# Kernel optimization log

Hardware: AMD Instinct MI355X
Metric: run time of the kernel (lower is better)

## Reference

```python
import jax, jax.numpy as jnp
import numpy as np

L, B, D, H = 2048, 2, 1024, 16
HD = D // H
DFF = 4 * D
EPS = 1e-5


def layernorm(x, g, b):
    mu = jnp.mean(x, axis=-1, keepdims=True)
    var = jnp.mean((x - mu) ** 2, axis=-1, keepdims=True)
    return (x - mu) * jax.lax.rsqrt(var + EPS) * g + b


def setup_inputs() -> dict:
    key = jax.random.key(0)
    ks = jax.random.split(key, 12)
    s = 0.02
    return {
        "x": jax.random.normal(ks[0], (L, B, D), jnp.float32),
        "ln1_g": jnp.ones((D,), jnp.float32),
        "ln1_b": jnp.zeros((D,), jnp.float32),
        "w_attn": jax.random.normal(ks[1], (D, 3 * D), jnp.float32) * s,
        "b_attn": jnp.zeros((3 * D,), jnp.float32),
        "w_proj": jax.random.normal(ks[2], (D, D), jnp.float32) * s,
        "b_proj": jnp.zeros((D,), jnp.float32),
        "ln2_g": jnp.ones((D,), jnp.float32),
        "ln2_b": jnp.zeros((D,), jnp.float32),
        "w_fc": jax.random.normal(ks[3], (D, DFF), jnp.float32) * s,
        "b_fc": jnp.zeros((DFF,), jnp.float32),
        "w_out": jax.random.normal(ks[4], (DFF, D), jnp.float32) * s,
        "b_out": jnp.zeros((D,), jnp.float32),
    }


def reference(x, ln1_g, ln1_b, w_attn, b_attn, w_proj, b_proj,
              ln2_g, ln2_b, w_fc, b_fc, w_out, b_out):
    # x: [L, B, D]
    h = layernorm(x, ln1_g, ln1_b)
    qkv = h @ w_attn + b_attn                     # [L, B, 3D]
    qkv = jnp.transpose(qkv, (1, 0, 2))            # [B, L, 3D]
    q, k, v = jnp.split(qkv, 3, axis=-1)

    def split_heads(t):                            # [B, L, D] -> [B, H, L, hd]
        return jnp.transpose(t.reshape(B, L, H, HD), (0, 2, 1, 3))

    q, k, v = split_heads(q), split_heads(k), split_heads(v)
    # present: stack of (key, value), key in [B,H,L,hd] layout (post transpose-back)
    present = jnp.stack((k, v))                    # [2, B, H, L, hd]

    scores = jnp.einsum('bhqd,bhkd->bhqk', q, k) / jnp.sqrt(jnp.float32(HD))
    w = jax.nn.softmax(scores, axis=-1)
    a = jnp.einsum('bhqk,bhkd->bhqd', w, v)        # [B, H, L, hd]
    a = jnp.transpose(a, (0, 2, 1, 3)).reshape(B, L, D)
    a = a @ w_proj + b_proj                        # [B, L, D]
    a = jnp.transpose(a, (1, 0, 2))                # [L, B, D]

    x = x + a
    m = jax.nn.gelu(layernorm(x, ln2_g, ln2_b) @ w_fc + b_fc) @ w_out + b_out
    x = x + m
    return x, present
```

## Files before the change

kernel.cpp:

```cpp
#include <hip/hip_runtime.h>
#include <stdint.h>

#define L_SEQ 2048
#define BATCH 2
#define DIM   1024
#define NH    16
#define HDIM  64
#define DFF_  4096
#define ROWS  (L_SEQ*BATCH)

#define QSCALE 0.18033688011112042f

typedef __attribute__((ext_vector_type(8))) short  bf16x8;
typedef __attribute__((ext_vector_type(4))) float  floatx4;

__device__ __forceinline__ unsigned short f2bf(float f) {
    union { float f; uint32_t u; } x; x.f = f;
    uint32_t r = x.u + 0x7fffu + ((x.u >> 16) & 1u);
    return (unsigned short)(r >> 16);
}
__device__ __forceinline__ float bf2f(unsigned short b) {
    union { uint32_t u; float f; } x; x.u = ((uint32_t)b) << 16;
    return x.f;
}
__device__ __forceinline__ uint32_t fbits(float f) {
    union { float f; uint32_t u; } x; x.f = f; return x.u;
}

__device__ __forceinline__ void load_lds16(const unsigned short* g, unsigned short* l) {
    __builtin_amdgcn_global_load_lds(
        (const __attribute__((address_space(1))) unsigned int*)g,
        (__attribute__((address_space(3))) unsigned int*)l, 16, 0, 0);
}

__global__ __launch_bounds__(256)
void transpose_all(const float* __restrict__ s0, unsigned short* __restrict__ d0,
                   const float* __restrict__ s1, unsigned short* __restrict__ d1,
                   const float* __restrict__ s2, unsigned short* __restrict__ d2,
                   const float* __restrict__ s3, unsigned short* __restrict__ d3)
{
    const int id = blockIdx.x;
    const float* src; unsigned short* dst; int K, N, local;
    if (id < 3072)      { src = s0; dst = d0; K = 1024; N = 3072; local = id; }
    else if (id < 4096) { src = s1; dst = d1; K = 1024; N = 1024; local = id - 3072; }
    else if (id < 8192) { src = s2; dst = d2; K = 1024; N = 4096; local = id - 4096; }
    else                { src = s3; dst = d3; K = 4096; N = 1024; local = id - 8192; }
    const int nN = N >> 5;
    const int bk = (local / nN) * 32, bn = (local % nN) * 32;

    __shared__ float tile[32][36];
    const int t = threadIdx.x;
    const int r = t >> 3, c4 = (t & 7) * 4;
    *(float4*)&tile[r][c4] = *(const float4*)(src + (size_t)(bk + r) * N + bn + c4);
    __syncthreads();
    ushort4 o;
    o.x = f2bf(tile[c4 + 0][r]);
    o.y = f2bf(tile[c4 + 1][r]);
    o.z = f2bf(tile[c4 + 2][r]);
    o.w = f2bf(tile[c4 + 3][r]);
    *(ushort4*)(dst + (size_t)(bn + r) * K + bk + c4) = o;
}

template<int INBF16>
__global__ __launch_bounds__(256)
void ln_rows(const void* __restrict__ xin, const float* __restrict__ g,
             const float* __restrict__ bta, unsigned short* __restrict__ out)
{
    const int row = blockIdx.x;
    const int t = threadIdx.x;
    float4 v;
    if (INBF16) {
        const ushort4 u = ((const ushort4*)((const unsigned short*)xin + (size_t)row * DIM))[t];
        v.x = bf2f(u.x); v.y = bf2f(u.y); v.z = bf2f(u.z); v.w = bf2f(u.w);
    } else {
        v = ((const float4*)((const float*)xin + (size_t)row * DIM))[t];
    }
    float s  = v.x + v.y + v.z + v.w;
    float s2 = v.x*v.x + v.y*v.y + v.z*v.z + v.w*v.w;
#pragma unroll
    for (int d = 1; d < 64; d <<= 1) { s += __shfl_xor(s, d, 64); s2 += __shfl_xor(s2, d, 64); }
    __shared__ float ss[4], ss2[4];
    const int w = t >> 6, lane = t & 63;
    if (lane == 0) { ss[w] = s; ss2[w] = s2; }
    __syncthreads();
    s  = ss[0] + ss[1] + ss[2] + ss[3];
    s2 = ss2[0] + ss2[1] + ss2[2] + ss2[3];
    const float mu   = s * (1.0f / DIM);
    const float var  = s2 * (1.0f / DIM) - mu * mu;
    const float rstd = rsqrtf(var + 1e-5f);
    const float4 gv = ((const float4*)g)[t];
    const float4 bv = ((const float4*)bta)[t];
    ushort4 o;
    o.x = f2bf((v.x - mu) * rstd * gv.x + bv.x);
    o.y = f2bf((v.y - mu) * rstd * gv.y + bv.y);
    o.z = f2bf((v.z - mu) * rstd * gv.z + bv.z);
    o.w = f2bf((v.w - mu) * rstd * gv.w + bv.w);
    *(ushort4*)(out + (size_t)row * DIM + t * 4) = o;
}

template<int GELU, int RESID, int OUTBF16, int MI>
__global__ __launch_bounds__(256)
void gemm_bt(const unsigned short* __restrict__ A,
             const unsigned short* __restrict__ Bt,
             const float* __restrict__ bias,
             const void* __restrict__ resid,
             void* __restrict__ outp,
             int M, int N, int K)
{
    __shared__ unsigned short As[MI * 32 * 32];
    __shared__ unsigned short Bs[128 * 32];
    const int t = threadIdx.x;
    const int w = t >> 6, lane = t & 63;
    const int quad = lane >> 4, l16 = lane & 15;
    const int wm = (w >> 1) * (MI * 16), wn = (w & 1) * 64;
    const int bm = blockIdx.x * (MI * 32), bn = blockIdx.y * 128;

    const int srow = lane >> 2;
    const int scol = (lane & 3) * 8;

    const unsigned short* Ab = A  + (size_t)bm * K;
    const unsigned short* Bb = Bt + (size_t)bn * K;

    floatx4 acc[MI][4] = {};

    for (int kc = 0; kc < K; kc += 32) {
        __syncthreads();
#pragma unroll
        for (int i = 0; i < MI / 2; ++i) {
            const int r0 = (i * 4 + w) * 16;
            load_lds16(Ab + (size_t)(r0 + srow) * K + kc + scol, As + r0 * 32);
        }
#pragma unroll
        for (int i = 0; i < 2; ++i) {
            const int r0 = (i * 4 + w) * 16;
            load_lds16(Bb + (size_t)(r0 + srow) * K + kc + scol, Bs + r0 * 32);
        }
        __syncthreads();
        bf16x8 af[MI], bf[4];
#pragma unroll
        for (int i = 0; i < MI; ++i) af[i] = *(const bf16x8*)(As + (wm + i*16 + l16) * 32 + quad * 8);
#pragma unroll
        for (int j = 0; j < 4; ++j) bf[j] = *(const bf16x8*)(Bs + (wn + j*16 + l16) * 32 + quad * 8);
#pragma unroll
        for (int i = 0; i < MI; ++i)
#pragma unroll
            for (int j = 0; j < 4; ++j)
                acc[i][j] = __builtin_amdgcn_mfma_f32_16x16x32_bf16(af[i], bf[j], acc[i][j], 0, 0, 0);
    }

#pragma unroll
    for (int i = 0; i < MI; ++i) {
#pragma unroll
        for (int j = 0; j < 4; ++j) {
            const int col = bn + wn + j*16 + l16;
            const float bv = bias[col];
#pragma unroll
            for (int r = 0; r < 4; ++r) {
                const int row = bm + wm + i*16 + quad*4 + r;
                float v = acc[i][j][r] + bv;
                if (RESID == 1) v += ((const float*)resid)[(size_t)row * N + col];
                if (RESID == 2) v += bf2f(((const unsigned short*)resid)[(size_t)row * N + col]);
                if (GELU) {
                    const float u = v;
                    float c = 2.302204225929898f * (u + 0.044715f * u * u * u);
                    c = fminf(c, 80.f);
                    const float e = exp2f(c);
                    v = u * (e / (1.0f + e));
                }
                if (OUTBF16) ((unsigned short*)outp)[(size_t)row * N + col] = f2bf(v);
                else         ((float*)outp)[(size_t)row * N + col] = v;
            }
        }
    }
}

__global__ __launch_bounds__(256)
void split_qkv(const unsigned short* __restrict__ qkv,
               unsigned short* __restrict__ q, unsigned short* __restrict__ k,
               float* __restrict__ present)
{
    const size_t idx = (size_t)blockIdx.x * 256 + threadIdx.x;
    const int g8  = idx & 7;
    const int l   = (idx >> 3) & 2047;
    const int bh  = (idx >> 14) & 31;
    const int sel = (int)(idx >> 19);
    const int b = bh >> 4, h = bh & 15;
    const unsigned short* src = qkv + (size_t)(l * BATCH + b) * (3 * DIM) + sel * DIM + h * HDIM + g8 * 8;
    const uint4 val = *(const uint4*)src;
    const unsigned short* sv = (const unsigned short*)&val;
    if (sel == 0) {
        unsigned short ov[8];
#pragma unroll
        for (int j = 0; j < 8; ++j) ov[j] = f2bf(bf2f(sv[j]) * QSCALE);
        *(uint4*)(q + ((size_t)bh * L_SEQ + l) * HDIM + g8 * 8) = *(uint4*)ov;
    } else {
        *(uint4*)(k + ((size_t)bh * L_SEQ + l) * HDIM + g8 * 8) = val;
        float* p = present + (((size_t)b * NH + h) * L_SEQ + l) * HDIM + (size_t)g8 * 8;
        float4 f0, f1;
        f0.x = bf2f(sv[0]); f0.y = bf2f(sv[1]); f0.z = bf2f(sv[2]); f0.w = bf2f(sv[3]);
        f1.x = bf2f(sv[4]); f1.y = bf2f(sv[5]); f1.z = bf2f(sv[6]); f1.w = bf2f(sv[7]);
        ((float4*)p)[0] = f0; ((float4*)p)[1] = f1;
    }
}

__global__ __launch_bounds__(256)
void transpose_v(const unsigned short* __restrict__ qkv, unsigned short* __restrict__ vt,
                 float* __restrict__ present)
{
    __shared__ unsigned short tile[64][72];
    const int lt = blockIdx.x;
    const int bh = blockIdx.y;
    const int b = bh >> 4, h = bh & 15;
    const int t = threadIdx.x;
#pragma unroll
    for (int i = 0; i < 2; ++i) {
        const int idx = i * 256 + t;
        const int l = idx >> 3, c = (idx & 7) * 8;
        const uint4 val =
            *(const uint4*)(qkv + (size_t)((lt * 64 + l) * BATCH + b) * (3 * DIM) + 2 * DIM + h * HDIM + c);
        *(uint4*)(&tile[l][c]) = val;
        const unsigned short* sv = (const unsigned short*)&val;
        float* p = present + ((((size_t)BATCH + b) * NH + h) * L_SEQ + lt * 64 + l) * HDIM + c;
        float4 f0, f1;
        f0.x = bf2f(sv[0]); f0.y = bf2f(sv[1]); f0.z = bf2f(sv[2]); f0.w = bf2f(sv[3]);
        f1.x = bf2f(sv[4]); f1.y = bf2f(sv[5]); f1.z = bf2f(sv[6]); f1.w = bf2f(sv[7]);
        ((float4*)p)[0] = f0; ((float4*)p)[1] = f1;
    }
    __syncthreads();
#pragma unroll
    for (int i = 0; i < 2; ++i) {
        const int idx = i * 256 + t;
        const int d = idx >> 3, l0 = (idx & 7) * 8;
        const int kk = l0 >> 3;
        ushort4 o[2];
        unsigned short* ov = (unsigned short*)o;
#pragma unroll
        for (int jj = 0; jj < 8; ++jj) {
            const int j = (jj + kk) & 7;
            ov[j] = tile[l0 + j][d];
        }
        *(uint4*)(vt + ((size_t)bh * HDIM + d) * L_SEQ + lt * 64 + l0) = *(uint4*)o;
    }
}

__global__ __launch_bounds__(256, 4)
void attn_kernel(const unsigned short* __restrict__ Q,
                 const unsigned short* __restrict__ Kk,
                 const unsigned short* __restrict__ Vt,
                 unsigned short* __restrict__ Opart,
                 float* __restrict__ Lpart)
{
    const int qt = blockIdx.x;
    const int ks = blockIdx.y;
    const int bh = blockIdx.z;
    const int b = bh >> 4, h = bh & 15;
    const int t = threadIdx.x, w = t >> 6, lane = t & 63;
    const int quad = lane >> 4, l16 = lane & 15;

    __shared__ unsigned short Ks[64][72];
    __shared__ unsigned short Vts[64][72];
    __shared__ unsigned short Ps[4][32][72];

    const size_t head_off = (size_t)bh * L_SEQ * HDIM;
    const int q_base = qt * 128 + w * 32;
    const int kt0 = ks * 1024;

    bf16x8 qf[2][2];
#pragma unroll
    for (int nf = 0; nf < 2; ++nf)
#pragma unroll
        for (int ds = 0; ds < 2; ++ds)
            qf[nf][ds] = *(const bf16x8*)(Q + head_off + (size_t)(q_base + nf*16 + l16) * HDIM + ds*32 + quad*8);

    const int sr = t >> 3;
    const int sc = (t & 7) * 8;

    floatx4 o[4][2] = {};
    float l_i[2] = {0.f, 0.f};

    for (int kt = kt0; kt < kt0 + 1024; kt += 64) {
        __syncthreads();
#pragma unroll
        for (int i = 0; i < 2; ++i) {
            const int row = sr + i * 32;
            *(uint4*)(&Ks[row][sc])  = *(const uint4*)(Kk + head_off + (size_t)(kt + row) * HDIM + sc);
            *(uint4*)(&Vts[row][sc]) = *(const uint4*)(Vt + head_off + (size_t)row * L_SEQ + kt + sc);
        }
        __syncthreads();

        floatx4 s[4][2] = {};
#pragma unroll
        for (int ds = 0; ds < 2; ++ds)
#pragma unroll
            for (int jt = 0; jt < 4; ++jt) {
                const bf16x8 kf = *(const bf16x8*)(&Ks[jt*16 + l16][ds*32 + quad*8]);
                s[jt][0] = __builtin_amdgcn_mfma_f32_16x16x32_bf16(kf, qf[0][ds], s[jt][0], 0, 0, 0);
                s[jt][1] = __builtin_amdgcn_mfma_f32_16x16x32_bf16(kf, qf[1][ds], s[jt][1], 0, 0, 0);
            }

#pragma unroll
        for (int nf = 0; nf < 2; ++nf)
#pragma unroll
            for (int jt = 0; jt < 4; ++jt) {
                const float p0 = exp2f(s[jt][nf][0]);
                const float p1 = exp2f(s[jt][nf][1]);
                const float p2 = exp2f(s[jt][nf][2]);
                const float p3 = exp2f(s[jt][nf][3]);
                l_i[nf] += (p0 + p1) + (p2 + p3);
                uint2 pk;
                pk.x = __builtin_amdgcn_perm(fbits(p1), fbits(p0), 0x07060302u);
                pk.y = __builtin_amdgcn_perm(fbits(p3), fbits(p2), 0x07060302u);
                *(uint2*)(&Ps[w][nf*16 + l16][jt*16 + quad*4]) = pk;
            }

#pragma unroll
        for (int kk = 0; kk < 2; ++kk) {
            const bf16x8 pf0 = *(const bf16x8*)(&Ps[w][l16]     [kk*32 + quad*8]);
            const bf16x8 pf1 = *(const bf16x8*)(&Ps[w][16 + l16][kk*32 + quad*8]);
#pragma unroll
            for (int dt = 0; dt < 4; ++dt) {
                const bf16x8 vf = *(const bf16x8*)(&Vts[dt*16 + l16][kk*32 + quad*8]);
                o[dt][0] = __builtin_amdgcn_mfma_f32_16x16x32_bf16(vf, pf0, o[dt][0], 0, 0, 0);
                o[dt][1] = __builtin_amdgcn_mfma_f32_16x16x32_bf16(vf, pf1, o[dt][1], 0, 0, 0);
            }
        }
    }

    unsigned short* Op = Opart + (size_t)ks * ROWS * DIM;
#pragma unroll
    for (int nf = 0; nf < 2; ++nf) {
        float l = l_i[nf];
        l += __shfl_xor(l, 16, 64);
        l += __shfl_xor(l, 32, 64);
        const int q = q_base + nf*16 + l16;
        if (quad == 0)
            Lpart[((size_t)ks * 32 + bh) * L_SEQ + q] = l;
#pragma unroll
        for (int dt = 0; dt < 4; ++dt) {
            ushort4 ov;
            ov.x = f2bf(o[dt][nf][0]); ov.y = f2bf(o[dt][nf][1]);
            ov.z = f2bf(o[dt][nf][2]); ov.w = f2bf(o[dt][nf][3]);
            *(ushort4*)(Op + (size_t)(q * BATCH + b) * DIM + h * HDIM + dt*16 + quad*4) = ov;
        }
    }
}

__global__ __launch_bounds__(256)
void attn_merge(const unsigned short* __restrict__ Opart,
                const float* __restrict__ Lpart,
                unsigned short* __restrict__ Aout)
{
    const int row = blockIdx.x;
    const int q = row >> 1, b = row & 1;
    const int t = threadIdx.x;
    const int col = t * 4;
    const int h = col >> 6;
    const int bh = b * 16 + h;
    const float l0 = Lpart[(size_t)bh * L_SEQ + q];
    const float l1 = Lpart[((size_t)32 + bh) * L_SEQ + q];
    const float inv = 1.0f / (l0 + l1);
    const ushort4 o0 = *(const ushort4*)(Opart + (size_t)row * DIM + col);
    const ushort4 o1 = *(const ushort4*)(Opart + (size_t)ROWS * DIM + (size_t)row * DIM + col);
    ushort4 ov;
    ov.x = f2bf((bf2f(o0.x) + bf2f(o1.x)) * inv);
    ov.y = f2bf((bf2f(o0.y) + bf2f(o1.y)) * inv);
    ov.z = f2bf((bf2f(o0.z) + bf2f(o1.z)) * inv);
    ov.w = f2bf((bf2f(o0.w) + bf2f(o1.w)) * inv);
    *(ushort4*)(Aout + (size_t)row * DIM + col) = ov;
}

extern "C" void kernel_launch(void* const* d_in, const int* in_sizes, int n_in,
                              void* d_out, int out_size, void* d_ws, size_t ws_size,
                              hipStream_t stream)
{
    const float* x      = (const float*)d_in[0];
    const float* ln1_g  = (const float*)d_in[1];
    const float* ln1_b  = (const float*)d_in[2];
    const float* w_attn = (const float*)d_in[3];
    const float* b_attn = (const float*)d_in[4];
    const float* w_proj = (const float*)d_in[5];
    const float* b_proj = (const float*)d_in[6];
    const float* ln2_g  = (const float*)d_in[7];
    const float* ln2_b  = (const float*)d_in[8];
    const float* w_fc   = (const float*)d_in[9];
    const float* b_fc   = (const float*)d_in[10];
    const float* w_out  = (const float*)d_in[11];
    const float* b_out  = (const float*)d_in[12];

    char* ws = (char*)d_ws;
    unsigned short* watT   = (unsigned short*)(ws + 0);
    unsigned short* wprojT = (unsigned short*)(ws + 6291456);
    unsigned short* wfcT   = (unsigned short*)(ws + 8388608);
    unsigned short* woutT  = (unsigned short*)(ws + 16777216);
    unsigned short* h      = (unsigned short*)(ws + 25165824);
    unsigned short* qkv    = (unsigned short*)(ws + 33554432);
    unsigned short* opart  = (unsigned short*)(ws + 33554432);
    float*          lpart  = (float*)(ws + 50331648);
    unsigned short* mws    = (unsigned short*)(ws + 33554432);
    unsigned short* qw     = (unsigned short*)(ws + 58720256);
    unsigned short* kw     = (unsigned short*)(ws + 67108864);
    unsigned short* vt     = (unsigned short*)(ws + 75497472);
    unsigned short* aw     = (unsigned short*)(ws + 83886080);
    unsigned short* x2     = (unsigned short*)(ws + 92274688);

    float* xout    = (float*)d_out;
    float* present = (float*)d_out + 4194304;

    transpose_all<<<12288, 256, 0, stream>>>(w_attn, watT, w_proj, wprojT, w_fc, wfcT, w_out, woutT);

    ln_rows<0><<<ROWS, 256, 0, stream>>>(x, ln1_g, ln1_b, h);
    gemm_bt<0,0,1,4><<<dim3(32, 24), 256, 0, stream>>>(h, watT, b_attn, nullptr, qkv, ROWS, 3*DIM, DIM);
    split_qkv<<<4096, 256, 0, stream>>>(qkv, qw, kw, present);
    transpose_v<<<dim3(32, 32), 256, 0, stream>>>(qkv, vt, present);
    attn_kernel<<<dim3(16, 2, 32), 256, 0, stream>>>(qw, kw, vt, opart, lpart);
    attn_merge<<<ROWS, 256, 0, stream>>>(opart, lpart, aw);
    gemm_bt<0,1,1,2><<<dim3(64, 8), 256, 0, stream>>>(aw, wprojT, b_proj, x, x2, ROWS, DIM, DIM);
    ln_rows<1><<<ROWS, 256, 0, stream>>>(x2, ln2_g, ln2_b, h);
    gemm_bt<1,0,1,4><<<dim3(32, 32), 256, 0, stream>>>(h, wfcT, b_fc, nullptr, mws, ROWS, DFF_, DIM);
    gemm_bt<0,2,0,2><<<dim3(64, 8), 256, 0, stream>>>(mws, woutT, b_out, x2, xout, ROWS, DIM, DFF_);
}
```

Measured before the change: 441.3 us.

## Split-K the MLP output GEMM with larger tiles and a reduction kernel

Adds a SPLITK template parameter to the bf16 MFMA GEMM so the K range can be split across blockIdx.z. For the final K=4096 output projection it switches to 128x128 tiles (MI=4) with two K-splits, keeping 512 blocks. The z=0 slice runs the normal bias and residual epilogue, while z=1 writes raw fp32 partials into a reused workspace buffer that a new splitk_add kernel then adds into the output. Larger tiles are meant to raise operand reuse per block, at the cost of an extra kernel launch and roughly 48 MB of additional fp32 partial-sum traffic.

New measurement: 418.6 us. -5.1%, faster.

```diff
diff --git a/kernel.cpp b/kernel.cpp
--- a/kernel.cpp
+++ b/kernel.cpp
@@ -98,13 +98,14 @@
     *(ushort4*)(out + (size_t)row * DIM + t * 4) = o;
 }
 
-template<int GELU, int RESID, int OUTBF16, int MI>
+template<int GELU, int RESID, int OUTBF16, int MI, int SPLITK>
 __global__ __launch_bounds__(256)
 void gemm_bt(const unsigned short* __restrict__ A,
              const unsigned short* __restrict__ Bt,
              const float* __restrict__ bias,
              const void* __restrict__ resid,
              void* __restrict__ outp,
+             float* __restrict__ part,
              int M, int N, int K)
 {
     __shared__ unsigned short As[MI * 32 * 32];
@@ -123,7 +124,10 @@
 
     floatx4 acc[MI][4] = {};
 
-    for (int kc = 0; kc < K; kc += 32) {
+    const int kspan = (SPLITK > 1) ? (K / SPLITK) : K;
+    const int k0    = (SPLITK > 1) ? blockIdx.z * kspan : 0;
+
+    for (int kc = k0; kc < k0 + kspan; kc += 32) {
         __syncthreads();
 #pragma unroll
         for (int i = 0; i < MI / 2; ++i) {
@@ -146,6 +150,22 @@
 #pragma unroll
             for (int j = 0; j < 4; ++j)
                 acc[i][j] = __builtin_amdgcn_mfma_f32_16x16x32_bf16(af[i], bf[j], acc[i][j], 0, 0, 0);
+    }
+
+    if (SPLITK > 1 && blockIdx.z > 0) {
+        float* po = part + (size_t)(blockIdx.z - 1) * ((size_t)M * N);
+#pragma unroll
+        for (int i = 0; i < MI; ++i)
+#pragma unroll
+            for (int j = 0; j < 4; ++j) {
+                const int col = bn + wn + j*16 + l16;
+#pragma unroll
+                for (int r = 0; r < 4; ++r) {
+                    const int row = bm + wm + i*16 + quad*4 + r;
+                    po[(size_t)row * N + col] = acc[i][j][r];
+                }
+            }
+        return;
     }
 
 #pragma unroll
@@ -172,6 +192,16 @@
             }
         }
     }
+}
+
+__global__ __launch_bounds__(256)
+void splitk_add(const float* __restrict__ part, float* __restrict__ outp)
+{
+    const size_t i = ((size_t)blockIdx.x * 256 + threadIdx.x) * 4;
+    float4 a = *(const float4*)(outp + i);
+    const float4 p = *(const float4*)(part + i);
+    a.x += p.x; a.y += p.y; a.z += p.z; a.w += p.w;
+    *(float4*)(outp + i) = a;
 }
 
 __global__ __launch_bounds__(256)
@@ -402,6 +432,7 @@
     unsigned short* vt     = (unsigned short*)(ws + 75497472);
     unsigned short* aw     = (unsigned short*)(ws + 83886080);
     unsigned short* x2     = (unsigned short*)(ws + 92274688);
+    float*          kpart  = (float*)(ws + 75497472);
 
     float* xout    = (float*)d_out;
     float* present = (float*)d_out + 4194304;
@@ -409,13 +440,14 @@
     transpose_all<<<12288, 256, 0, stream>>>(w_attn, watT, w_proj, wprojT, w_fc, wfcT, w_out, woutT);
 
     ln_rows<0><<<ROWS, 256, 0, stream>>>(x, ln1_g, ln1_b, h);
-    gemm_bt<0,0,1,4><<<dim3(32, 24), 256, 0, stream>>>(h, watT, b_attn, nullptr, qkv, ROWS, 3*DIM, DIM);
+    gemm_bt<0,0,1,4,1><<<dim3(32, 24), 256, 0, stream>>>(h, watT, b_attn, nullptr, qkv, nullptr, ROWS, 3*DIM, DIM);
     split_qkv<<<4096, 256, 0, stream>>>(qkv, qw, kw, present);
     transpose_v<<<dim3(32, 32), 256, 0, stream>>>(qkv, vt, present);
     attn_kernel<<<dim3(16, 2, 32), 256, 0, stream>>>(qw, kw, vt, opart, lpart);
     attn_merge<<<ROWS, 256, 0, stream>>>(opart, lpart, aw);
-    gemm_bt<0,1,1,2><<<dim3(64, 8), 256, 0, stream>>>(aw, wprojT, b_proj, x, x2, ROWS, DIM, DIM);
+    gemm_bt<0,1,1,2,1><<<dim3(64, 8), 256, 0, stream>>>(aw, wprojT, b_proj, x, x2, nullptr, ROWS, DIM, DIM);
     ln_rows<1><<<ROWS, 256, 0, stream>>>(x2, ln2_g, ln2_b, h);
-    gemm_bt<1,0,1,4><<<dim3(32, 32), 256, 0, stream>>>(h, wfcT, b_fc, nullptr, mws, ROWS, DFF_, DIM);
-    gemm_bt<0,2,0,2><<<dim3(64, 8), 256, 0, stream>>>(mws, woutT, b_out, x2, xout, ROWS, DIM, DFF_);
-}
+    gemm_bt<1,0,1,4,1><<<dim3(32, 32), 256, 0, stream>>>(h, wfcT, b_fc, nullptr, mws, nullptr, ROWS, DFF_, DIM);
+    gemm_bt<0,2,0,4,2><<<dim3(32, 8, 2), 256, 0, stream>>>(mws, woutT, b_out, x2, xout, kpart, ROWS, DIM, DFF_);
+    splitk_add<<<4096, 256, 0, stream>>>(kpart, xout);
+}
```
